# Performance work log

Hardware: AMD Instinct MI355X
Metric: run time of the kernel (lower is better)

Reference implementation:

```python
import jax, jax.numpy as jnp
import numpy as np
import math

EMBED = 768
HEADS = 12
HEAD_DIM = EMBED // HEADS

def setup_inputs() -> dict:
    key = jax.random.key(0)
    ks = jax.random.split(key, 9)
    B, T, C = 32, 1024, EMBED
    s = 1.0 / math.sqrt(C)
    return {
        "hidden_states": jax.random.normal(ks[0], (B, T, C), dtype=jnp.float32),
        "q_w": jax.random.normal(ks[1], (C, C), dtype=jnp.float32) * s,
        "q_b": jnp.zeros((C,), dtype=jnp.float32),
        "k_w": jax.random.normal(ks[2], (C, C), dtype=jnp.float32) * s,
        "k_b": jnp.zeros((C,), dtype=jnp.float32),
        "v_w": jax.random.normal(ks[3], (C, C), dtype=jnp.float32) * s,
        "v_b": jnp.zeros((C,), dtype=jnp.float32),
        "o_w": jax.random.normal(ks[4], (C, C), dtype=jnp.float32) * s,
        "o_b": jnp.zeros((C,), dtype=jnp.float32),
    }

def reference(hidden_states, q_w, q_b, k_w, k_b, v_w, v_b, o_w, o_b):
    B, T, C = hidden_states.shape
    H, D = HEADS, C // HEADS
    # Linear: x @ W^T + b (torch nn.Linear convention); here weights stored (C, C)
    q = (hidden_states @ q_w.T + q_b).reshape(B, T, H, D).transpose(0, 2, 1, 3)
    k = (hidden_states @ k_w.T + k_b).reshape(B, T, H, D).transpose(0, 2, 1, 3)
    v = (hidden_states @ v_w.T + v_b).reshape(B, T, H, D).transpose(0, 2, 1, 3)
    scale = 1.0 / math.sqrt(D)
    scores = jnp.einsum("bhqd,bhkd->bhqk", q, k) * scale
    attn = jax.nn.softmax(scores, axis=-1)
    out = jnp.einsum("bhqk,bhkd->bhqd", attn, v)  # (B,H,T,D)
    out = out.transpose(0, 2, 1, 3).reshape(B, T, C)
    return out @ o_w.T + o_b
```

## Files before the change

kernel.cpp:

```cpp
#include <hip/hip_runtime.h>
#include <hip/hip_bf16.h>

#define B_ 32
#define T_ 1024
#define C_ 768
#define H_ 12
#define D_ 64
#define BT_ (B_*T_)
#define CC_ (C_*C_)

typedef __attribute__((ext_vector_type(4))) float f32x4;
typedef __attribute__((ext_vector_type(8))) short bf16x8;
typedef __attribute__((ext_vector_type(4))) short short4_t;
typedef __attribute__((ext_vector_type(2))) unsigned int u32x2;
typedef unsigned short u16;
typedef unsigned int u32;

#define QSCALE 0.1803368801111244f

__device__ __forceinline__ float bf2f(u16 u){
  union { float f; unsigned int i; } v; v.i = ((unsigned int)u)<<16; return v.f;
}
__device__ __forceinline__ u16 f2bf(float f){
  union { float f; unsigned int i; } v; v.f = f;
  return (u16)((v.i + 0x7fffu + ((v.i>>16)&1u)) >> 16);
}
__device__ __forceinline__ u32 pack2bf(float lo, float hi){
  union { float f; u32 i; } a, b; a.f = lo; b.f = hi;
  return ((a.i + 0x8000u) >> 16) | ((b.i + 0x8000u) & 0xFFFF0000u);
}
__device__ __forceinline__ void split2(float f, u16& h, u16& l){
  h = f2bf(f);
  l = f2bf(f - bf2f(h));
}

__device__ __forceinline__ void gll16(const void* g, void* l){
  __builtin_amdgcn_global_load_lds(
      (const __attribute__((address_space(1))) u32*)g,
      (__attribute__((address_space(3))) u32*)l, 16, 0, 0);
}

__global__ void sentinel_kernel(float* out, int n){
  int i = blockIdx.x*blockDim.x + threadIdx.x;
  if (i < n) out[i] = 12345.0f;
}

__global__ void xquant_kernel(const float* __restrict__ x, u16* __restrict__ xb, int n8){
  int i = blockIdx.x*blockDim.x + threadIdx.x;
  int stride = gridDim.x*blockDim.x;
  for (; i < n8; i += stride) {
    f32x4 a = *(const f32x4*)(x + (size_t)i*8);
    f32x4 b = *(const f32x4*)(x + (size_t)i*8 + 4);
    bf16x8 o;
    #pragma unroll
    for (int j = 0; j < 4; ++j) { o[j] = (short)f2bf(a[j]); o[j+4] = (short)f2bf(b[j]); }
    *(bf16x8*)(xb + (size_t)i*8) = o;
  }
}

__global__ void wquant_kernel(const float* __restrict__ qw, const float* __restrict__ kw,
                              const float* __restrict__ vw, const float* __restrict__ ow,
                              u16* __restrict__ W3b, u16* __restrict__ Wohi,
                              u16* __restrict__ Wolo){
  int i = (blockIdx.x*blockDim.x + threadIdx.x)*4;
  if (i >= CC_) return;
  f32x4 q = *(const f32x4*)(qw+i);
  f32x4 k = *(const f32x4*)(kw+i);
  f32x4 v = *(const f32x4*)(vw+i);
  f32x4 o = *(const f32x4*)(ow+i);
  short4_t tq, tk, tv, th, tl;
  #pragma unroll
  for (int j = 0; j < 4; ++j) {
    tq[j] = (short)f2bf(q[j]);
    tk[j] = (short)f2bf(k[j]);
    tv[j] = (short)f2bf(v[j]);
    u16 hh, ll; split2(o[j], hh, ll);
    th[j] = (short)hh; tl[j] = (short)ll;
  }
  *(short4_t*)(W3b + i)          = tq;
  *(short4_t*)(W3b + CC_ + i)    = tk;
  *(short4_t*)(W3b + 2*CC_ + i)  = tv;
  *(short4_t*)(Wohi + i)         = th;
  *(short4_t*)(Wolo + i)         = tl;
}

template<int MODE>
__global__ __launch_bounds__(256,2)
void gemm_glds(const u16* __restrict__ Ab, const u16* __restrict__ Wb,
               const u16* __restrict__ Wlo_,
               const float* __restrict__ bq, const float* __restrict__ bk,
               const float* __restrict__ bv,
               u16* __restrict__ Qb, u16* __restrict__ Kb, u16* __restrict__ Vb,
               float* __restrict__ Out)
{
  __shared__ __align__(1024) u16 sA[128*64];
  __shared__ __align__(1024) u16 sB[128*64];
  __shared__ __align__(1024) u16 sBl[MODE==1 ? 128*64 : 8];
  const int tid = threadIdx.x;
  const int lane = tid & 63;
  const int l15 = lane & 15, l16 = lane >> 4;
  const int wave = tid >> 6;
  const int wr = wave >> 1, wc = wave & 1;

  const int bid = blockIdx.x;
  const int xcd = bid & 7;
  const int idx = bid >> 3;
  int z, nb, mloc;
  if (MODE == 0) { z = idx % 3; int r = idx / 3; nb = r % 6; mloc = r / 6; }
  else           { z = 0; nb = idx % 6; mloc = idx / 6; }
  const int m0 = (xcd*32 + mloc) * 128;
  const int n0 = nb * 128;
  const u16* W = (MODE==0) ? (Wb + (size_t)z*CC_) : Wb;
  const float* bias = (MODE==1) ? bq : (z==0 ? bq : (z==1 ? bk : bv));

  const int lrow = lane >> 3;
  const int cbyte = ((lane & 7) ^ lrow) << 4;

  f32x4 acc[4][4];
  #pragma unroll
  for (int i=0;i<4;++i)
    #pragma unroll
    for (int j=0;j<4;++j)
      acc[i][j] = (f32x4){0.f,0.f,0.f,0.f};

  for (int k0 = 0; k0 < C_; k0 += 64) {
    __syncthreads();
    #pragma unroll
    for (int sg = 0; sg < 4; ++sg) {
      int seg = wave*4 + sg;
      int row = seg*8 + lrow;
      gll16((const char*)(Ab + (size_t)(m0+row)*C_ + k0) + cbyte, sA + seg*512);
      gll16((const char*)(W  + (size_t)(n0+row)*C_ + k0) + cbyte, sB + seg*512);
      if (MODE == 1)
        gll16((const char*)(Wlo_ + (size_t)(n0+row)*C_ + k0) + cbyte, sBl + seg*512);
    }
    asm volatile("s_waitcnt vmcnt(0)" ::: "memory");
    __syncthreads();

    #pragma unroll
    for (int kc = 0; kc < 2; ++kc) {
      bf16x8 a[4], bh[4], bl[4];
      #pragma unroll
      for (int mf = 0; mf < 4; ++mf) {
        int row = wr*64 + mf*16 + l15;
        int off = (row<<7) + ((kc*64 + l16*16) ^ ((row&7)<<4));
        a[mf] = *(const bf16x8*)((const char*)sA + off);
      }
      #pragma unroll
      for (int nf = 0; nf < 4; ++nf) {
        int row = wc*64 + nf*16 + l15;
        int off = (row<<7) + ((kc*64 + l16*16) ^ ((row&7)<<4));
        bh[nf] = *(const bf16x8*)((const char*)sB + off);
        if (MODE == 1) bl[nf] = *(const bf16x8*)((const char*)sBl + off);
      }
      #pragma unroll
      for (int mf = 0; mf < 4; ++mf)
        #pragma unroll
        for (int nf = 0; nf < 4; ++nf) {
          acc[mf][nf] = __builtin_amdgcn_mfma_f32_16x16x32_bf16(a[mf], bh[nf], acc[mf][nf],0,0,0);
          if (MODE == 1)
            acc[mf][nf] = __builtin_amdgcn_mfma_f32_16x16x32_bf16(a[mf], bl[nf], acc[mf][nf],0,0,0);
        }
    }
  }

  #pragma unroll
  for (int mf = 0; mf < 4; ++mf) {
    #pragma unroll
    for (int nf = 0; nf < 4; ++nf) {
      int mgb = m0 + wr*64 + mf*16 + l16*4;
      int ng  = n0 + wc*64 + nf*16 + l15;
      float bv = bias[ng];
      if (MODE == 1) {
        #pragma unroll
        for (int r = 0; r < 4; ++r)
          Out[(size_t)(mgb+r)*C_ + ng] = acc[mf][nf][r] + bv;
      } else {
        int b = mgb >> 10, t0 = mgb & 1023;
        int h = ng >> 6, d = ng & 63;
        int bh_ = b*H_ + h;
        if (z == 2) {
          short4_t vh;
          #pragma unroll
          for (int r = 0; r < 4; ++r)
            vh[r] = (short)f2bf(acc[mf][nf][r] + bv);
          size_t idx2 = ((size_t)bh_*D_ + d)*T_ + t0;
          *(short4_t*)&Vb[idx2] = vh;
        } else {
          u16* dst = (z==0) ? Qb : Kb;
          float scale = (z==0) ? QSCALE : 1.0f;
          #pragma unroll
          for (int r = 0; r < 4; ++r) {
            size_t idx2 = ((size_t)bh_*T_ + (t0+r))*D_ + d;
            dst[idx2] = f2bf((acc[mf][nf][r] + bv) * scale);
          }
        }
      }
    }
  }
}

__global__ __launch_bounds__(256,2)
void attn_kernel(const u16* __restrict__ Qb, const u16* __restrict__ Kb,
                 const u16* __restrict__ Vb, u16* __restrict__ AOb)
{
  __shared__ __align__(16) u16 sK[64*64];
  __shared__ __align__(16) u16 sV[64*64];
  __shared__ __align__(16) u32 sP[4][32*32];
  const int tid = threadIdx.x;
  const int lane = tid & 63;
  const int l15 = lane & 15, l16 = lane >> 4;
  const int wave = tid >> 6;
  const int bid = blockIdx.x;
  const int sw  = (bid & 7) * 384 + (bid >> 3);
  const int bh  = sw >> 3;
  const int q0  = (sw & 7) * 128 + wave * 32;

  bf16x8 qh[2][2];
  #pragma unroll
  for (int mf = 0; mf < 2; ++mf)
    #pragma unroll
    for (int kc = 0; kc < 2; ++kc)
      qh[mf][kc] = *(const bf16x8*)(Qb + ((size_t)bh*T_ + q0 + mf*16 + l15)*D_ + kc*32 + l16*8);

  f32x4 o[2][4];
  #pragma unroll
  for (int mf = 0; mf < 2; ++mf)
    #pragma unroll
    for (int i = 0; i < 4; ++i) o[mf][i] = (f32x4){0.f,0.f,0.f,0.f};
  float l_r[2] = {0.f, 0.f};

  const size_t kbase = (size_t)bh * (T_*D_);
  const size_t vbase = (size_t)bh * (D_*T_);
  u32* pw = sP[wave];

  int srow[2], sdst[2], scolb[2];
  #pragma unroll
  for (int iss = 0; iss < 2; ++iss) {
    int oo = (iss*256 + tid)*16;
    srow[iss]  = oo >> 7;
    scolb[iss] = oo & 127;
    sdst[iss]  = (srow[iss]<<7) | (scolb[iss] ^ ((srow[iss]&7)<<4));
  }
  bf16x8 kreg[2], vreg[2];
  #pragma unroll
  for (int iss = 0; iss < 2; ++iss) {
    kreg[iss] = *(const bf16x8*)((const char*)(Kb + kbase + (size_t)srow[iss]*D_) + scolb[iss]);
    vreg[iss] = *(const bf16x8*)((const char*)(Vb + vbase + (size_t)srow[iss]*T_) + scolb[iss]);
  }

  for (int kt = 0; kt < T_/64; ++kt) {
    __syncthreads();
    #pragma unroll
    for (int iss = 0; iss < 2; ++iss) {
      *(bf16x8*)((char*)sK + sdst[iss]) = kreg[iss];
      *(bf16x8*)((char*)sV + sdst[iss]) = vreg[iss];
    }
    if (kt + 1 < T_/64) {
      #pragma unroll
      for (int iss = 0; iss < 2; ++iss) {
        kreg[iss] = *(const bf16x8*)((const char*)(Kb + kbase + (size_t)((kt+1)*64+srow[iss])*D_) + scolb[iss]);
        vreg[iss] = *(const bf16x8*)((const char*)(Vb + vbase + (size_t)srow[iss]*T_ + (kt+1)*64) + scolb[iss]);
      }
    }
    __syncthreads();

    f32x4 s[2][4];
    #pragma unroll
    for (int mf = 0; mf < 2; ++mf)
      #pragma unroll
      for (int nf = 0; nf < 4; ++nf) s[mf][nf] = (f32x4){0.f,0.f,0.f,0.f};
    __builtin_amdgcn_s_setprio(1);
    #pragma unroll
    for (int nf = 0; nf < 4; ++nf) {
      #pragma unroll
      for (int kc = 0; kc < 2; ++kc) {
        int row = nf*16 + l15;
        int off = (row<<7) | (((kc*64) + l16*16) ^ ((row&7)<<4));
        bf16x8 kf = *(const bf16x8*)((const char*)sK + off);
        s[0][nf] = __builtin_amdgcn_mfma_f32_16x16x32_bf16(kf, qh[0][kc], s[0][nf],0,0,0);
        s[1][nf] = __builtin_amdgcn_mfma_f32_16x16x32_bf16(kf, qh[1][kc], s[1][nf],0,0,0);
      }
    }
    __builtin_amdgcn_s_setprio(0);

    #pragma unroll
    for (int mf = 0; mf < 2; ++mf) {
      int q = mf*16 + l15;
      u32* prow = pw + q*32;
      int swz = (q & 7) << 2;
      #pragma unroll
      for (int nf = 0; nf < 4; ++nf) {
        float p0 = __builtin_amdgcn_exp2f(s[mf][nf][0]);
        float p1 = __builtin_amdgcn_exp2f(s[mf][nf][1]);
        float p2 = __builtin_amdgcn_exp2f(s[mf][nf][2]);
        float p3 = __builtin_amdgcn_exp2f(s[mf][nf][3]);
        l_r[mf] += (p0 + p1) + (p2 + p3);
        u32x2 w2;
        w2[0] = pack2bf(p0, p1);
        w2[1] = pack2bf(p2, p3);
        *(u32x2*)(prow + ((8*nf + 2*l16) ^ swz)) = w2;
      }
    }

    __builtin_amdgcn_s_setprio(1);
    #pragma unroll
    for (int kc = 0; kc < 2; ++kc) {
      bf16x8 pf[2];
      #pragma unroll
      for (int mf = 0; mf < 2; ++mf) {
        int q = mf*16 + l15;
        pf[mf] = *(const bf16x8*)(pw + q*32 + ((kc*16 + l16*4) ^ ((q&7)<<2)));
      }
      #pragma unroll
      for (int df = 0; df < 4; ++df) {
        int row = df*16 + l15;
        int offv = (row<<7) | (((kc*64) + l16*16) ^ ((row&7)<<4));
        bf16x8 vf = *(const bf16x8*)((const char*)sV + offv);
        o[0][df] = __builtin_amdgcn_mfma_f32_16x16x32_bf16(pf[0], vf, o[0][df],0,0,0);
        o[1][df] = __builtin_amdgcn_mfma_f32_16x16x32_bf16(pf[1], vf, o[1][df],0,0,0);
      }
    }
    __builtin_amdgcn_s_setprio(0);
  }

  #pragma unroll
  for (int mf = 0; mf < 2; ++mf) {
    float t = l_r[mf];
    t += __shfl_xor(t, 16);
    t += __shfl_xor(t, 32);
    l_r[mf] = t;
  }

  const int b = bh / H_, h = bh % H_;
  #pragma unroll
  for (int mf = 0; mf < 2; ++mf)
    #pragma unroll
    for (int r = 0; r < 4; ++r) {
      float inv = 1.0f / __shfl(l_r[mf], (l16 << 2) + r);
      int t = q0 + mf*16 + l16*4 + r;
      size_t rowb = ((size_t)(b*T_ + t))*C_ + h*D_;
      #pragma unroll
      for (int df = 0; df < 4; ++df)
        AOb[rowb + df*16 + l15] = f2bf(o[mf][df][r] * inv);
    }
}

extern "C" void kernel_launch(void* const* d_in, const int* in_sizes, int n_in,
                              void* d_out, int out_size, void* d_ws, size_t ws_size,
                              hipStream_t stream) {
  const float* X  = (const float*)d_in[0];
  const float* qw = (const float*)d_in[1];
  const float* qb = (const float*)d_in[2];
  const float* kw = (const float*)d_in[3];
  const float* kb = (const float*)d_in[4];
  const float* vw = (const float*)d_in[5];
  const float* vb = (const float*)d_in[6];
  const float* ow = (const float*)d_in[7];
  const float* ob = (const float*)d_in[8];
  float* out = (float*)d_out;

  const size_t SZ = (size_t)BT_*C_*sizeof(u16);
  const size_t NEED = 4*SZ + 5*(size_t)CC_*sizeof(u16);
  if (ws_size < NEED) {
    sentinel_kernel<<<(out_size+255)/256,256,0,stream>>>(out, out_size);
    return;
  }
  char* ws = (char*)d_ws;
  u16* Qb   = (u16*)(ws + 0*SZ);
  u16* Kb   = (u16*)(ws + 1*SZ);
  u16* Vb   = (u16*)(ws + 2*SZ);
  u16* AOb  = (u16*)(ws + 3*SZ);
  u16* W3b  = (u16*)(ws + 4*SZ);
  u16* Wohi = W3b + 3*(size_t)CC_;
  u16* Wolo = Wohi + (size_t)CC_;
  u16* Xb   = AOb;

  wquant_kernel<<<CC_/4/256,256,0,stream>>>(qw, kw, vw, ow, W3b, Wohi, Wolo);
  xquant_kernel<<<2048,256,0,stream>>>(X, Xb, BT_*C_/8);
  gemm_glds<0><<<4608,256,0,stream>>>(Xb, W3b, nullptr, qb, kb, vb,
      Qb, Kb, Vb, nullptr);
  attn_kernel<<<3072,256,0,stream>>>(Qb, Kb, Vb, AOb);
  gemm_glds<1><<<1536,256,0,stream>>>(AOb, Wohi, Wolo, ob, nullptr, nullptr,
      nullptr, nullptr, nullptr, out);
}
```

Before: 362.3 us.

## Rewrite QKV GEMM with 256x256 tiles, double-buffered LDS and interleaved MFMA phases

Replaces the templated QKV projection GEMM with a dedicated 512-thread kernel that computes 256x256 output tiles. It double-buffers the A and B tiles in LDS and splits each K step into four MFMA quadrants, interleaving the async global-to-LDS loads for the next step with compute and raising wave priority around the MFMA blocks. The larger tile increases operand reuse and cuts global traffic per FLOP, and the prefetching hides load latency behind compute. The cost is one block per CU with 128KB of LDS and a high accumulator register count, which lowers occupancy. The output projection GEMM is split into its own non-templated kernel with unchanged logic.

```diff
diff --git a/kernel.cpp b/kernel.cpp
--- a/kernel.cpp
+++ b/kernel.cpp
@@ -84,18 +84,184 @@
   *(short4_t*)(Wolo + i)         = tl;
 }
 
-template<int MODE>
+__global__ __launch_bounds__(512,1)
+void gemm_qkv(const u16* __restrict__ Ab, const u16* __restrict__ Wb,
+              const float* __restrict__ bq, const float* __restrict__ bk,
+              const float* __restrict__ bv,
+              u16* __restrict__ Qb, u16* __restrict__ Kb, u16* __restrict__ Vb)
+{
+  __shared__ __align__(1024) u16 sA[2][256*64];
+  __shared__ __align__(1024) u16 sB[2][256*64];
+  const int tid = threadIdx.x;
+  const int lane = tid & 63;
+  const int l15 = lane & 15, l16 = lane >> 4;
+  const int wave = tid >> 6;
+  const int wm = wave >> 2, wn = wave & 3;
+  const int bid = blockIdx.x;
+  const int xcd = bid & 7;
+  const int idx = bid >> 3;
+  const int mloc = idx / 9, nb = idx % 9;
+  const int m0 = (xcd*16 + mloc) * 256;
+  const int n0 = nb * 256;
+  const int z  = nb / 3;
+  const float* bias = (z==0) ? bq : (z==1 ? bk : bv);
+
+  const int lrow = lane >> 3;
+  const int cbyte = ((lane & 7) ^ lrow) << 4;
+
+  f32x4 acc[8][4];
+  #pragma unroll
+  for (int i=0;i<8;++i)
+    #pragma unroll
+    for (int j=0;j<4;++j)
+      acc[i][j] = (f32x4){0.f,0.f,0.f,0.f};
+
+  auto stageA = [&](int c, int kt){
+    #pragma unroll
+    for (int i=0;i<4;++i){
+      int row = i*64 + wave*8 + lrow;
+      gll16((const char*)(Ab + (size_t)(m0+row)*C_ + kt*64) + cbyte,
+            sA[c] + (i*64 + wave*8)*64);
+    }
+  };
+  auto stageB = [&](int c, int kt){
+    #pragma unroll
+    for (int i=0;i<4;++i){
+      int row = i*64 + wave*8 + lrow;
+      gll16((const char*)(Wb + (size_t)(n0+row)*C_ + kt*64) + cbyte,
+            sB[c] + (i*64 + wave*8)*64);
+    }
+  };
+
+  stageA(0,0); stageB(0,0);
+  asm volatile("s_waitcnt vmcnt(0)" ::: "memory");
+  __syncthreads();
+
+  for (int t = 0; t < 12; ++t) {
+    const int c = t & 1;
+    const u16* Atile = sA[c];
+    const u16* Btile = sB[c];
+    bf16x8 aLo[4][2], aHi[4][2], bLo[2][2], bHi[2][2];
+
+    if (t < 11) stageA(c^1, t+1);
+    #pragma unroll
+    for (int mf=0; mf<4; ++mf)
+      #pragma unroll
+      for (int kc=0; kc<2; ++kc){
+        int row = wm*128 + mf*16 + l15;
+        aLo[mf][kc] = *(const bf16x8*)((const char*)Atile + row*128 + ((kc*64 + l16*16) ^ ((row&7)<<4)));
+      }
+    #pragma unroll
+    for (int nf=0; nf<2; ++nf)
+      #pragma unroll
+      for (int kc=0; kc<2; ++kc){
+        int row = wn*64 + nf*16 + l15;
+        bLo[nf][kc] = *(const bf16x8*)((const char*)Btile + row*128 + ((kc*64 + l16*16) ^ ((row&7)<<4)));
+      }
+    __builtin_amdgcn_sched_barrier(0);
+    __builtin_amdgcn_s_setprio(1);
+    #pragma unroll
+    for (int mf=0; mf<4; ++mf)
+      #pragma unroll
+      for (int nf=0; nf<2; ++nf)
+        #pragma unroll
+        for (int kc=0; kc<2; ++kc)
+          acc[mf][nf] = __builtin_amdgcn_mfma_f32_16x16x32_bf16(aLo[mf][kc], bLo[nf][kc], acc[mf][nf],0,0,0);
+    __builtin_amdgcn_s_setprio(0);
+    __builtin_amdgcn_sched_barrier(0);
+
+    if (t < 11) stageB(c^1, t+1);
+    #pragma unroll
+    for (int nf=0; nf<2; ++nf)
+      #pragma unroll
+      for (int kc=0; kc<2; ++kc){
+        int row = wn*64 + (nf+2)*16 + l15;
+        bHi[nf][kc] = *(const bf16x8*)((const char*)Btile + row*128 + ((kc*64 + l16*16) ^ ((row&7)<<4)));
+      }
+    __builtin_amdgcn_sched_barrier(0);
+    __builtin_amdgcn_s_setprio(1);
+    #pragma unroll
+    for (int mf=0; mf<4; ++mf)
+      #pragma unroll
+      for (int nf=0; nf<2; ++nf)
+        #pragma unroll
+        for (int kc=0; kc<2; ++kc)
+          acc[mf][nf+2] = __builtin_amdgcn_mfma_f32_16x16x32_bf16(aLo[mf][kc], bHi[nf][kc], acc[mf][nf+2],0,0,0);
+    __builtin_amdgcn_s_setprio(0);
+    __builtin_amdgcn_sched_barrier(0);
+
+    #pragma unroll
+    for (int mf=0; mf<4; ++mf)
+      #pragma unroll
+      for (int kc=0; kc<2; ++kc){
+        int row = wm*128 + (mf+4)*16 + l15;
+        aHi[mf][kc] = *(const bf16x8*)((const char*)Atile + row*128 + ((kc*64 + l16*16) ^ ((row&7)<<4)));
+      }
+    __builtin_amdgcn_sched_barrier(0);
+    __builtin_amdgcn_s_setprio(1);
+    #pragma unroll
+    for (int mf=0; mf<4; ++mf)
+      #pragma unroll
+      for (int nf=0; nf<2; ++nf)
+        #pragma unroll
+        for (int kc=0; kc<2; ++kc)
+          acc[mf+4][nf+2] = __builtin_amdgcn_mfma_f32_16x16x32_bf16(aHi[mf][kc], bHi[nf][kc], acc[mf+4][nf+2],0,0,0);
+    __builtin_amdgcn_s_setprio(0);
+    __builtin_amdgcn_sched_barrier(0);
+
+    __builtin_amdgcn_s_setprio(1);
+    #pragma unroll
+    for (int mf=0; mf<4; ++mf)
+      #pragma unroll
+      for (int nf=0; nf<2; ++nf)
+        #pragma unroll
+        for (int kc=0; kc<2; ++kc)
+          acc[mf+4][nf] = __builtin_amdgcn_mfma_f32_16x16x32_bf16(aHi[mf][kc], bLo[nf][kc], acc[mf+4][nf],0,0,0);
+    __builtin_amdgcn_s_setprio(0);
+    if (t < 11) {
+      asm volatile("s_waitcnt vmcnt(0)" ::: "memory");
+      __syncthreads();
+    }
+  }
+
+  #pragma unroll
+  for (int mf = 0; mf < 8; ++mf) {
+    #pragma unroll
+    for (int nf = 0; nf < 4; ++nf) {
+      int mgb = m0 + wm*128 + mf*16 + l16*4;
+      int ngz = (nb%3)*256 + wn*64 + nf*16 + l15;
+      float bv = bias[ngz];
+      int b = mgb >> 10, t0 = mgb & 1023;
+      int h = ngz >> 6, d = ngz & 63;
+      int bh_ = b*H_ + h;
+      if (z == 2) {
+        short4_t vh;
+        #pragma unroll
+        for (int r = 0; r < 4; ++r)
+          vh[r] = (short)f2bf(acc[mf][nf][r] + bv);
+        size_t idx2 = ((size_t)bh_*D_ + d)*T_ + t0;
+        *(short4_t*)&Vb[idx2] = vh;
+      } else {
+        u16* dst = (z==0) ? Qb : Kb;
+        float scale = (z==0) ? QSCALE : 1.0f;
+        #pragma unroll
+        for (int r = 0; r < 4; ++r) {
+          size_t idx2 = ((size_t)bh_*T_ + (t0+r))*D_ + d;
+          dst[idx2] = f2bf((acc[mf][nf][r] + bv) * scale);
+        }
+      }
+    }
+  }
+}
+
 __global__ __launch_bounds__(256,2)
-void gemm_glds(const u16* __restrict__ Ab, const u16* __restrict__ Wb,
-               const u16* __restrict__ Wlo_,
-               const float* __restrict__ bq, const float* __restrict__ bk,
-               const float* __restrict__ bv,
-               u16* __restrict__ Qb, u16* __restrict__ Kb, u16* __restrict__ Vb,
-               float* __restrict__ Out)
+void gemm_out(const u16* __restrict__ Ab, const u16* __restrict__ Whi,
+              const u16* __restrict__ Wlo_, const float* __restrict__ bo,
+              float* __restrict__ Out)
 {
   __shared__ __align__(1024) u16 sA[128*64];
   __shared__ __align__(1024) u16 sB[128*64];
-  __shared__ __align__(1024) u16 sBl[MODE==1 ? 128*64 : 8];
+  __shared__ __align__(1024) u16 sBl[128*64];
   const int tid = threadIdx.x;
   const int lane = tid & 63;
   const int l15 = lane & 15, l16 = lane >> 4;
@@ -105,13 +271,9 @@
   const int bid = blockIdx.x;
   const int xcd = bid & 7;
   const int idx = bid >> 3;
-  int z, nb, mloc;
-  if (MODE == 0) { z = idx % 3; int r = idx / 3; nb = r % 6; mloc = r / 6; }
-  else           { z = 0; nb = idx % 6; mloc = idx / 6; }
+  const int nb = idx % 6, mloc = idx / 6;
   const int m0 = (xcd*32 + mloc) * 128;
   const int n0 = nb * 128;
-  const u16* W = (MODE==0) ? (Wb + (size_t)z*CC_) : Wb;
-  const float* bias = (MODE==1) ? bq : (z==0 ? bq : (z==1 ? bk : bv));
 
   const int lrow = lane >> 3;
   const int cbyte = ((lane & 7) ^ lrow) << 4;
@@ -129,10 +291,9 @@
     for (int sg = 0; sg < 4; ++sg) {
       int seg = wave*4 + sg;
       int row = seg*8 + lrow;
-      gll16((const char*)(Ab + (size_t)(m0+row)*C_ + k0) + cbyte, sA + seg*512);
-      gll16((const char*)(W  + (size_t)(n0+row)*C_ + k0) + cbyte, sB + seg*512);
-      if (MODE == 1)
-        gll16((const char*)(Wlo_ + (size_t)(n0+row)*C_ + k0) + cbyte, sBl + seg*512);
+      gll16((const char*)(Ab   + (size_t)(m0+row)*C_ + k0) + cbyte, sA  + seg*512);
+      gll16((const char*)(Whi  + (size_t)(n0+row)*C_ + k0) + cbyte, sB  + seg*512);
+      gll16((const char*)(Wlo_ + (size_t)(n0+row)*C_ + k0) + cbyte, sBl + seg*512);
     }
     asm volatile("s_waitcnt vmcnt(0)" ::: "memory");
     __syncthreads();
@@ -151,15 +312,14 @@
         int row = wc*64 + nf*16 + l15;
         int off = (row<<7) + ((kc*64 + l16*16) ^ ((row&7)<<4));
         bh[nf] = *(const bf16x8*)((const char*)sB + off);
-        if (MODE == 1) bl[nf] = *(const bf16x8*)((const char*)sBl + off);
+        bl[nf] = *(const bf16x8*)((const char*)sBl + off);
       }
       #pragma unroll
       for (int mf = 0; mf < 4; ++mf)
         #pragma unroll
         for (int nf = 0; nf < 4; ++nf) {
           acc[mf][nf] = __builtin_amdgcn_mfma_f32_16x16x32_bf16(a[mf], bh[nf], acc[mf][nf],0,0,0);
-          if (MODE == 1)
-            acc[mf][nf] = __builtin_amdgcn_mfma_f32_16x16x32_bf16(a[mf], bl[nf], acc[mf][nf],0,0,0);
+          acc[mf][nf] = __builtin_amdgcn_mfma_f32_16x16x32_bf16(a[mf], bl[nf], acc[mf][nf],0,0,0);
         }
     }
   }
@@ -170,32 +330,10 @@
     for (int nf = 0; nf < 4; ++nf) {
       int mgb = m0 + wr*64 + mf*16 + l16*4;
       int ng  = n0 + wc*64 + nf*16 + l15;
-      float bv = bias[ng];
-      if (MODE == 1) {
-        #pragma unroll
-        for (int r = 0; r < 4; ++r)
-          Out[(size_t)(mgb+r)*C_ + ng] = acc[mf][nf][r] + bv;
-      } else {
-        int b = mgb >> 10, t0 = mgb & 1023;
-        int h = ng >> 6, d = ng & 63;
-        int bh_ = b*H_ + h;
-        if (z == 2) {
-          short4_t vh;
-          #pragma unroll
-          for (int r = 0; r < 4; ++r)
-            vh[r] = (short)f2bf(acc[mf][nf][r] + bv);
-          size_t idx2 = ((size_t)bh_*D_ + d)*T_ + t0;
-          *(short4_t*)&Vb[idx2] = vh;
-        } else {
-          u16* dst = (z==0) ? Qb : Kb;
-          float scale = (z==0) ? QSCALE : 1.0f;
-          #pragma unroll
-          for (int r = 0; r < 4; ++r) {
-            size_t idx2 = ((size_t)bh_*T_ + (t0+r))*D_ + d;
-            dst[idx2] = f2bf((acc[mf][nf][r] + bv) * scale);
-          }
-        }
-      }
+      float bv = bo[ng];
+      #pragma unroll
+      for (int r = 0; r < 4; ++r)
+        Out[(size_t)(mgb+r)*C_ + ng] = acc[mf][nf][r] + bv;
     }
   }
 }
@@ -378,9 +516,7 @@
 
   wquant_kernel<<<CC_/4/256,256,0,stream>>>(qw, kw, vw, ow, W3b, Wohi, Wolo);
   xquant_kernel<<<2048,256,0,stream>>>(X, Xb, BT_*C_/8);
-  gemm_glds<0><<<4608,256,0,stream>>>(Xb, W3b, nullptr, qb, kb, vb,
-      Qb, Kb, Vb, nullptr);
+  gemm_qkv<<<1152,512,0,stream>>>(Xb, W3b, qb, kb, vb, Qb, Kb, Vb);
   attn_kernel<<<3072,256,0,stream>>>(Qb, Kb, Vb, AOb);
-  gemm_glds<1><<<1536,256,0,stream>>>(AOb, Wohi, Wolo, ob, nullptr, nullptr,
-      nullptr, nullptr, nullptr, out);
-}
+  gemm_out<<<1536,256,0,stream>>>(AOb, Wohi, Wolo, ob, out);
+}
```

After: 386.5 us. +6.7%, slower.
